# Kernel optimization log

Hardware: AMD Instinct MI355X
Metric: run time of the kernel (lower is better)

## Reference

```python
import jax, jax.numpy as jnp
import numpy as np

B, T = 128, 64
N_IN, H1, H2, N_OUT = 2048, 2048, 1024, 128
BETA = 0.95
THRESH = 1.0  # snn.Leaky default threshold


def spike(x):
    # Heaviside firing function (forward of snntorch ATan surrogate)
    return (x > 0).astype(x.dtype)


def setup_inputs() -> dict:
    key = jax.random.key(0)
    ks = jax.random.split(key, 5)

    def linear_params(k, fan_in, fan_out):
        k1, k2 = jax.random.split(k)
        bound = 1.0 / np.sqrt(fan_in)  # torch nn.Linear default init
        W = jax.random.uniform(k1, (fan_out, fan_in), minval=-bound, maxval=bound, dtype=jnp.float32)
        b = jax.random.uniform(k2, (fan_out,), minval=-bound, maxval=bound, dtype=jnp.float32)
        return W, b

    W0, b0 = linear_params(ks[0], N_IN, N_IN)
    W1, b1 = linear_params(ks[1], N_IN, H1)
    W2, b2 = linear_params(ks[2], H1, H2)
    W3, b3 = linear_params(ks[3], H2, N_OUT)
    x = jax.random.normal(ks[4], (B, T, N_IN), dtype=jnp.float32)
    return {"x": x, "W0": W0, "b0": b0, "W1": W1, "b1": b1,
            "W2": W2, "b2": b2, "W3": W3, "b3": b3}


def _lif(cur, mem):
    # snntorch Leaky (reset_mechanism='subtract'): reset computed from incoming mem
    reset = spike(mem - THRESH)
    mem_new = BETA * mem + cur - reset * THRESH
    spk = spike(mem_new - THRESH)
    return spk, mem_new


def reference(x, W0, b0, W1, b1, W2, b2, W3, b3):
    Bb = x.shape[0]
    dt = x.dtype
    mems0 = (jnp.zeros((Bb, N_IN), dt), jnp.zeros((Bb, H1), dt),
             jnp.zeros((Bb, H2), dt), jnp.zeros((Bb, N_OUT), dt))
    x_tbf = jnp.swapaxes(x, 0, 1)  # [T, B, N_IN]

    def step(carry, x_t):
        m0, m1, m2, m3 = carry
        s0, m0 = _lif(x_t @ W0.T + b0, m0)
        s1, m1 = _lif(s0 @ W1.T + b1, m1)
        s2, m2 = _lif(s1 @ W2.T + b2, m2)
        s3, m3 = _lif(s2 @ W3.T + b3, m3)
        return (m0, m1, m2, m3), (s3, m3)

    _, (spk3, mem3) = jax.lax.scan(step, mems0, x_tbf)
    # [T, B, N_OUT] -> [B, T, N_OUT]
    return jnp.swapaxes(spk3, 0, 1), jnp.swapaxes(mem3, 0, 1)
```

## Files before the change

### kernel.cpp

```cpp
#include <hip/hip_runtime.h>
#include <cstddef>
#include <cstdint>


#define BETA 0.95f

static constexpr int B_ = 128;
static constexpr int T_ = 64;
static constexpr int M_ = B_ * T_;
static constexpr int NOUT = 128;

typedef __bf16 bf16x8 __attribute__((ext_vector_type(8)));
typedef _Float16 f16x8 __attribute__((ext_vector_type(8)));
typedef float f32x4 __attribute__((ext_vector_type(4)));
typedef ushort u16x8 __attribute__((ext_vector_type(8)));

__device__ __forceinline__ ushort f32_bf16_rne(float f) {
  uint32_t u = __float_as_uint(f);
  uint32_t r = u + 0x7FFFu + ((u >> 16) & 1u);
  return (ushort)(r >> 16);
}
__device__ __forceinline__ float bf16_f32(ushort h) {
  return __uint_as_float(((uint32_t)h) << 16);
}
__device__ __forceinline__ ushort h2u(_Float16 h) {
  union { _Float16 h; ushort u; } v; v.h = h; return v.u;
}
__device__ __forceinline__ _Float16 u2h(ushort u) {
  union { ushort u; _Float16 h; } v; v.u = u; return v.h;
}

__global__ __launch_bounds__(256) void split2_f16(
    const float* __restrict__ S, ushort* __restrict__ oh,
    ushort* __restrict__ ol, int K, int nslots)
{
  int g = blockIdx.x * 256 + threadIdx.x;
  if (g >= nslots) return;
  int spr = K >> 3;
  int row = g / spr;
  int sl = g - row * spr;
  int kb = sl >> 3;
  int slot = sl & 7;
  int pslot = (slot & 4) | ((slot & 3) ^ ((row >> 1) & 3));
  const float* src = S + (size_t)row * K + (kb << 6) + (slot << 3);
  size_t dst = (size_t)row * K + (kb << 6) + (pslot << 3);
  u16x8 vh, vl;
#pragma unroll
  for (int i = 0; i < 8; ++i) {
    float f = src[i];
    _Float16 h = (_Float16)f;
    float hf = (float)h;
    if (fabsf(hf) < 6.103515625e-05f) { h = (_Float16)0.0f; hf = 0.0f; }
    float l = (f - hf) * 4096.0f;
    vh[i] = h2u(h);
    vl[i] = h2u((_Float16)l);
  }
  *reinterpret_cast<u16x8*>(oh + dst) = vh;
  *reinterpret_cast<u16x8*>(ol + dst) = vl;
}

__global__ __launch_bounds__(256) void split3_swz(
    const float* __restrict__ S, ushort* __restrict__ o1,
    ushort* __restrict__ o2, ushort* __restrict__ o3,
    int K, int nslots)
{
  int g = blockIdx.x * 256 + threadIdx.x;
  if (g >= nslots) return;
  int spr = K >> 3;
  int row = g / spr;
  int sl = g - row * spr;
  int kb = sl >> 3;
  int slot = sl & 7;
  int pslot = slot ^ (row & 7);
  const float* src = S + (size_t)row * K + (kb << 6) + (slot << 3);
  size_t dst = (size_t)row * K + (kb << 6) + (pslot << 3);
  u16x8 v1, v2, v3;
#pragma unroll
  for (int i = 0; i < 8; ++i) {
    float f = src[i];
    ushort h1 = f32_bf16_rne(f);
    float r = f - bf16_f32(h1);
    ushort h2 = f32_bf16_rne(r);
    float r2 = r - bf16_f32(h2);
    ushort h3 = f32_bf16_rne(r2);
    v1[i] = h1; v2[i] = h2; v3[i] = h3;
  }
  *reinterpret_cast<u16x8*>(o1 + dst) = v1;
  *reinterpret_cast<u16x8*>(o2 + dst) = v2;
  *reinterpret_cast<u16x8*>(o3 + dst) = v3;
}

template<int NP, int FMT>
__global__ __launch_bounds__(512) void gemm_mainL(
    const ushort* __restrict__ A0p, const ushort* __restrict__ A1p,
    const ushort* __restrict__ Bh0, const ushort* __restrict__ Bl0,
    const ushort* __restrict__ Bh1, const ushort* __restrict__ Bl1,
    int K, int N,
    const float* __restrict__ bias, ushort* __restrict__ spk)
{
  __shared__ __align__(16) ushort lds[67584];

  const int tid = threadIdx.x;
  const int lane = tid & 63;
  const int wid = tid >> 6;
  const int wm = wid >> 1;
  const int wn = wid & 1;
  const int lane15 = lane & 15;
  const int lhi = lane >> 4;
  const int sg2 = lhi ^ ((lane15 >> 1) & 3);

  int nwg = gridDim.x * gridDim.y;
  int bid = blockIdx.y * gridDim.x + blockIdx.x;
  int cpx = nwg >> 3;
  int sw = (bid & 7) * cpx + (bid >> 3);
  int bx = sw % gridDim.x, by = sw / gridDim.x;
  const int bm = by * 256, bn = bx * 128;

  const int sr2 = tid >> 2;
  const int sg = tid & 3;

  const ushort* Aps[2] = {A0p, (NP == 2) ? A1p : A0p};
  const ushort* Bhs[2] = {Bh0, (NP == 2) ? Bh1 : Bh0};
  const ushort* Bls[2] = {Bl0, (NP == 2) ? Bl1 : Bl0};

  auto stage = [&](int t1, int h, int d) {
    const int pn = t1 >> 5;
    const int k0 = (t1 & 31) * 64 + h * 32;
    const ushort* Ap = Aps[pn];
#pragma unroll
    for (int l = 0; l < 2; ++l) {
      int row = sr2 + l * 128;
      __builtin_amdgcn_global_load_lds(
          (const __attribute__((address_space(1))) void*)(Ap + (size_t)(bm + row) * K + k0 + sg * 8),
          (__attribute__((address_space(3))) void*)(lds + d * 16384 + h * 8192 + row * 32 + sg * 8),
          16, 0, 0);
    }
#pragma unroll
    for (int s = 0; s < 2; ++s) {
      const ushort* Bp = (s == 0) ? Bhs[pn] : Bls[pn];
      __builtin_amdgcn_global_load_lds(
          (const __attribute__((address_space(1))) void*)(Bp + (size_t)(bn + sr2) * K + k0 + sg * 8),
          (__attribute__((address_space(3))) void*)(lds + 32768 + ((d * 2 + h) * 2 + s) * 4096 + sr2 * 32 + sg * 8),
          16, 0, 0);
    }
  };

  f32x4 accM[4][4], accC[4][4];
#pragma unroll
  for (int i = 0; i < 4; ++i)
#pragma unroll
    for (int j = 0; j < 4; ++j) {
      accM[i][j] = (f32x4){0.f, 0.f, 0.f, 0.f};
      accC[i][j] = (f32x4){0.f, 0.f, 0.f, 0.f};
    }

  const int NT = NP * 32;

  stage(0, 0, 0);
  stage(0, 1, 0);
  asm volatile("s_waitcnt vmcnt(0)" ::: "memory");
  asm volatile("s_barrier" ::: "memory");

  for (int t = 0; t < NT; ++t) {
    const int d = t & 1;
    const int p = t >> 5;
    const int nb = (NP == 2 && p == 1) ? 1 : 2;
#pragma unroll
    for (int h = 0; h < 2; ++h) {
      f16x8 af[4];
      const ushort* Ab = lds + (d * 2 + h) * 8192;
#pragma unroll
      for (int i = 0; i < 4; ++i)
        af[i] = *(const f16x8*)(Ab + (wm * 64 + i * 16 + lane15) * 32 + sg2 * 8);

      if (t < NT - 1) {
        stage(t + 1, h, d ^ 1);
        asm volatile("s_waitcnt vmcnt(4)" ::: "memory");
      } else if (h == 0) {
        asm volatile("s_waitcnt vmcnt(0)" ::: "memory");
      }
      asm volatile("s_barrier" ::: "memory");

      __builtin_amdgcn_s_setprio(1);
#pragma unroll
      for (int s = 0; s < 2; ++s) {
        if (s < nb) {
          const ushort* Bb = lds + 32768 + ((d * 2 + h) * 2 + s) * 4096;
          f16x8 bf[4];
#pragma unroll
          for (int j = 0; j < 4; ++j)
            bf[j] = *(const f16x8*)(Bb + (wn * 64 + j * 16 + lane15) * 32 + sg2 * 8);
          if (p == 0 && s == 0) {
#pragma unroll
            for (int i = 0; i < 4; ++i)
#pragma unroll
              for (int j = 0; j < 4; ++j)
                accM[i][j] = __builtin_amdgcn_mfma_f32_16x16x32_f16(af[i], bf[j], accM[i][j], 0, 0, 0);
          } else {
#pragma unroll
            for (int i = 0; i < 4; ++i)
#pragma unroll
              for (int j = 0; j < 4; ++j)
                accC[i][j] = __builtin_amdgcn_mfma_f32_16x16x32_f16(af[i], bf[j], accC[i][j], 0, 0, 0);
          }
        }
      }
      __builtin_amdgcn_s_setprio(0);
      asm volatile("s_barrier" ::: "memory");
    }
  }

  asm volatile("s_waitcnt vmcnt(0)" ::: "memory");
  __syncthreads();

  float* curb = (float*)lds;
#pragma unroll
  for (int i = 0; i < 4; ++i) {
    int rl = wm * 64 + i * 16 + lhi * 4;
#pragma unroll
    for (int j = 0; j < 4; ++j) {
      int cl = wn * 64 + j * 16 + lane15;
      f32x4 vm = accM[i][j], vc = accC[i][j];
#pragma unroll
      for (int r = 0; r < 4; ++r)
        curb[(rl + r) * 132 + cl] = __fmaf_rn(vc[r], 2.44140625e-4f, vm[r]);
    }
  }
  __syncthreads();

  {
    int b2 = tid >> 7;
    int n = tid & 127;
    int cg = bn + n;
    float bv = bias[cg];
    int nb6 = cg >> 6;
    int sl = (cg >> 3) & 7;
    int nlow = cg & 7;
    const ushort one = FMT ? (ushort)0x3C00 : (ushort)0x3F80;
    float mem = 0.f;
    for (int t2 = 0; t2 < 64; ++t2) {
      float c = __fadd_rn(curb[(b2 * 64 + t2) * 132 + n], bv);
      float reset = ((mem - 1.0f) > 0.0f) ? 1.0f : 0.0f;
      mem = __fmul_rn(BETA, mem);
      mem = __fadd_rn(mem, c);
      mem = __fadd_rn(mem, -reset);
      ushort sv = ((mem - 1.0f) > 0.0f) ? one : (ushort)0;
      int m = bm + b2 * 64 + t2;
      int ps = FMT ? ((sl & 4) | ((sl & 3) ^ ((m >> 1) & 3)))
                   : (sl ^ (m & 7));
      spk[(size_t)m * N + (nb6 << 6) + (ps << 3) + nlow] = sv;
    }
  }
}

__global__ __launch_bounds__(256) void gemm_seg_lif(
    const ushort* __restrict__ A0,
    const ushort* __restrict__ B0, const ushort* __restrict__ B1,
    const ushort* __restrict__ B2,
    const float* __restrict__ bias,
    float* __restrict__ spk_out, float* __restrict__ mem_out)
{
  __shared__ ushort As[128 * 64];
  __shared__ ushort Bs[128 * 64];
  __shared__ float curb[128 * 132];

  const int tid = threadIdx.x;
  const int lane = tid & 63;
  const int wid = tid >> 6;
  const int wr = wid >> 1, wc = wid & 1;
  const int lane15 = lane & 15;
  const int lhi = lane >> 4;
  const int rswz = lane15 & 7;
  const int lrow = lane >> 3, lslot = lane & 7;

  int nwg = gridDim.x * gridDim.y;
  int bid = blockIdx.y * gridDim.x + blockIdx.x;
  int cpx = nwg >> 3;
  int sw = (bid & 7) * cpx + (bid >> 3);
  int bx = sw % gridDim.x, by = sw / gridDim.x;
  const int bm = by * 128, bn = bx * 128;

  f32x4 accM[4][4], accC[4][4];
#pragma unroll
  for (int i = 0; i < 4; ++i)
#pragma unroll
    for (int j = 0; j < 4; ++j) {
      accM[i][j] = (f32x4){0.f, 0.f, 0.f, 0.f};
      accC[i][j] = (f32x4){0.f, 0.f, 0.f, 0.f};
    }

  const bool isA = (wid < 2);
  ushort* lbase = isA ? As : Bs;
  const int rowbase0 = isA ? bm : bn;
  const int chunk0 = (wid & 1) * 8;

  for (int p = 0; p < 3; ++p) {
    const ushort* Bp = (p == 0) ? B0 : ((p == 1) ? B1 : B2);
    const ushort* gsrc = isA ? A0 : Bp;
    for (int k0 = 0; k0 < 1024; k0 += 64) {
      __syncthreads();
#pragma unroll
      for (int c = 0; c < 8; ++c) {
        int chunk = chunk0 + c;
        int row = chunk * 8 + lrow;
        const ushort* g = gsrc + (size_t)(rowbase0 + row) * 1024 + k0 + (lslot << 3);
        __builtin_amdgcn_global_load_lds(
            (const __attribute__((address_space(1))) void*)(g),
            (__attribute__((address_space(3))) void*)(lbase + chunk * 512),
            16, 0, 0);
      }
      __syncthreads();
#pragma unroll
      for (int kk = 0; kk < 2; ++kk) {
        int sp = ((kk << 2) | lhi) ^ rswz;
        bf16x8 af[4], bg[4];
#pragma unroll
        for (int i = 0; i < 4; ++i)
          af[i] = *(const bf16x8*)(As + (wr * 64 + i * 16 + lane15) * 64 + sp * 8);
#pragma unroll
        for (int j = 0; j < 4; ++j)
          bg[j] = *(const bf16x8*)(Bs + (wc * 64 + j * 16 + lane15) * 64 + sp * 8);
        if (p == 0) {
#pragma unroll
          for (int i = 0; i < 4; ++i)
#pragma unroll
            for (int j = 0; j < 4; ++j)
              accM[i][j] = __builtin_amdgcn_mfma_f32_16x16x32_bf16(af[i], bg[j], accM[i][j], 0, 0, 0);
        } else {
#pragma unroll
          for (int i = 0; i < 4; ++i)
#pragma unroll
            for (int j = 0; j < 4; ++j)
              accC[i][j] = __builtin_amdgcn_mfma_f32_16x16x32_bf16(af[i], bg[j], accC[i][j], 0, 0, 0);
        }
      }
    }
  }

  __syncthreads();
#pragma unroll
  for (int j = 0; j < 4; ++j) {
    int cl = wc * 64 + j * 16 + lane15;
#pragma unroll
    for (int i = 0; i < 4; ++i) {
      int rl = wr * 64 + i * 16 + lhi * 4;
      f32x4 vm = accM[i][j], vc = accC[i][j];
#pragma unroll
      for (int r = 0; r < 4; ++r)
        curb[(rl + r) * 132 + cl] = vm[r] + vc[r];
    }
  }
  __syncthreads();

  {
    int b2 = tid >> 7;
    int n = tid & 127;
    float bv = bias[bn + n];
    float mem = 0.f;
    for (int t2 = 0; t2 < 64; ++t2) {
      float c = __fadd_rn(curb[(b2 * 64 + t2) * 132 + n], bv);
      float reset = ((mem - 1.0f) > 0.0f) ? 1.0f : 0.0f;
      mem = __fmul_rn(BETA, mem);
      mem = __fadd_rn(mem, c);
      mem = __fadd_rn(mem, -reset);
      int m = bm + b2 * 64 + t2;
      size_t idx = (size_t)m * 128 + bn + n;
      spk_out[idx] = ((mem - 1.0f) > 0.0f) ? 1.0f : 0.0f;
      mem_out[idx] = mem;
    }
  }
}

extern "C" void kernel_launch(void* const* d_in, const int* in_sizes, int n_in,
                              void* d_out, int out_size, void* d_ws, size_t ws_size,
                              hipStream_t stream)
{
  const float* x  = (const float*)d_in[0];
  const float* W0 = (const float*)d_in[1];
  const float* b0 = (const float*)d_in[2];
  const float* W1 = (const float*)d_in[3];
  const float* b1 = (const float*)d_in[4];
  const float* W2 = (const float*)d_in[5];
  const float* b2 = (const float*)d_in[6];
  const float* W3 = (const float*)d_in[7];
  const float* b3 = (const float*)d_in[8];
  float* out = (float*)d_out;

  char* ws = (char*)d_ws;
  size_t off = 0;
  auto take = [&](size_t bytes) -> char* {
    char* p = ws + off;
    off += (bytes + 255) & ~(size_t)255;
    return p;
  };

  ushort* w0h = (ushort*)take((size_t)2048 * 2048 * 2);
  ushort* w0l = (ushort*)take((size_t)2048 * 2048 * 2);
  ushort* w1h = (ushort*)take((size_t)2048 * 2048 * 2);
  ushort* w1l = (ushort*)take((size_t)2048 * 2048 * 2);
  ushort* w2h = (ushort*)take((size_t)1024 * 2048 * 2);
  ushort* w2l = (ushort*)take((size_t)1024 * 2048 * 2);
  ushort* w3s[3];
  for (int i = 0; i < 3; ++i) w3s[i] = (ushort*)take((size_t)128 * 1024 * 2);
  ushort* xh = (ushort*)take((size_t)M_ * 2048 * 2);
  ushort* xl = (ushort*)take((size_t)M_ * 2048 * 2);
  ushort* s0 = (ushort*)take((size_t)M_ * 2048 * 2);
  ushort* s1 = xh;
  ushort* s2 = xl;

  dim3 blk(256);
  dim3 fblk(512);

  {
    int ns = 2048 * 2048 / 8;
    split2_f16<<<(ns + 255) / 256, blk, 0, stream>>>(W0, w0h, w0l, 2048, ns);
    split2_f16<<<(ns + 255) / 256, blk, 0, stream>>>(W1, w1h, w1l, 2048, ns);
    ns = 1024 * 2048 / 8;
    split2_f16<<<(ns + 255) / 256, blk, 0, stream>>>(W2, w2h, w2l, 2048, ns);
    ns = 128 * 1024 / 8;
    split3_swz<<<(ns + 255) / 256, blk, 0, stream>>>(W3, w3s[0], w3s[1], w3s[2], 1024, ns);
    ns = M_ * 2048 / 8;
    split2_f16<<<(ns + 255) / 256, blk, 0, stream>>>(x, xh, xl, 2048, ns);
  }

  {
    dim3 grid(2048 / 128, M_ / 256);
    gemm_mainL<2, 1><<<grid, fblk, 0, stream>>>(
        xh, xl, w0h, w0l, w0h, w0h, 2048, 2048, b0, s0);
  }
  {
    dim3 grid(2048 / 128, M_ / 256);
    gemm_mainL<1, 1><<<grid, fblk, 0, stream>>>(
        s0, s0, w1h, w1l, w1h, w1l, 2048, 2048, b1, s1);
  }
  {
    dim3 grid(1024 / 128, M_ / 256);
    gemm_mainL<1, 0><<<grid, fblk, 0, stream>>>(
        s1, s1, w2h, w2l, w2h, w2l, 2048, 1024, b2, s2);
  }
  {
    float* spk3 = out;
    float* mem3 = out + (size_t)M_ * NOUT;
    gemm_seg_lif<<<dim3(1, 64), blk, 0, stream>>>(s2, w3s[0], w3s[1], w3s[2], b3, spk3, mem3);
  }
}
```

Baseline: 478.0 us.

## Double-buffer LDS fragment reads in registers to overlap with MFMA

Restructures the GEMM main loop so the A/B fragments for the next half-tile are read from LDS into a second register set while MFMAs run on the current set. Each k-step is unrolled into two explicit halves with ping-pong fragment arrays, and the first fragments are preloaded before the loop. The aim is to hide LDS read latency behind matrix math. The cost is a larger live register set (two full fragment buffers on top of 128 accumulator registers), which may reduce occupancy or cause spills. There is also one redundant fragment read on the final iteration.

```diff
diff --git a/kernel.cpp b/kernel.cpp
--- a/kernel.cpp
+++ b/kernel.cpp
@@ -145,6 +145,22 @@
     }
   };
 
+  auto read_af = [&](int dd, int hh, f16x8* af) {
+    const ushort* Ab = lds + (dd * 2 + hh) * 8192;
+#pragma unroll
+    for (int i = 0; i < 4; ++i)
+      af[i] = *(const f16x8*)(Ab + (wm * 64 + i * 16 + lane15) * 32 + sg2 * 8);
+  };
+  auto read_bf = [&](int dd, int hh, f16x8* bf) {
+#pragma unroll
+    for (int s = 0; s < 2; ++s) {
+      const ushort* Bb = lds + 32768 + ((dd * 2 + hh) * 2 + s) * 4096;
+#pragma unroll
+      for (int j = 0; j < 4; ++j)
+        bf[s * 4 + j] = *(const f16x8*)(Bb + (wn * 64 + j * 16 + lane15) * 32 + sg2 * 8);
+    }
+  };
+
   f32x4 accM[4][4], accC[4][4];
 #pragma unroll
   for (int i = 0; i < 4; ++i)
@@ -161,53 +177,74 @@
   asm volatile("s_waitcnt vmcnt(0)" ::: "memory");
   asm volatile("s_barrier" ::: "memory");
 
+  f16x8 afA[4], bfA[8], afB[4], bfB[8];
+  read_af(0, 0, afA);
+  read_bf(0, 0, bfA);
+
   for (int t = 0; t < NT; ++t) {
     const int d = t & 1;
     const int p = t >> 5;
     const int nb = (NP == 2 && p == 1) ? 1 : 2;
-#pragma unroll
-    for (int h = 0; h < 2; ++h) {
-      f16x8 af[4];
-      const ushort* Ab = lds + (d * 2 + h) * 8192;
-#pragma unroll
-      for (int i = 0; i < 4; ++i)
-        af[i] = *(const f16x8*)(Ab + (wm * 64 + i * 16 + lane15) * 32 + sg2 * 8);
-
-      if (t < NT - 1) {
-        stage(t + 1, h, d ^ 1);
-        asm volatile("s_waitcnt vmcnt(4)" ::: "memory");
-      } else if (h == 0) {
-        asm volatile("s_waitcnt vmcnt(0)" ::: "memory");
-      }
-      asm volatile("s_barrier" ::: "memory");
-
-      __builtin_amdgcn_s_setprio(1);
-#pragma unroll
-      for (int s = 0; s < 2; ++s) {
-        if (s < nb) {
-          const ushort* Bb = lds + 32768 + ((d * 2 + h) * 2 + s) * 4096;
-          f16x8 bf[4];
-#pragma unroll
-          for (int j = 0; j < 4; ++j)
-            bf[j] = *(const f16x8*)(Bb + (wn * 64 + j * 16 + lane15) * 32 + sg2 * 8);
-          if (p == 0 && s == 0) {
-#pragma unroll
-            for (int i = 0; i < 4; ++i)
-#pragma unroll
-              for (int j = 0; j < 4; ++j)
-                accM[i][j] = __builtin_amdgcn_mfma_f32_16x16x32_f16(af[i], bf[j], accM[i][j], 0, 0, 0);
-          } else {
-#pragma unroll
-            for (int i = 0; i < 4; ++i)
-#pragma unroll
-              for (int j = 0; j < 4; ++j)
-                accC[i][j] = __builtin_amdgcn_mfma_f32_16x16x32_f16(af[i], bf[j], accC[i][j], 0, 0, 0);
-          }
+
+    if (t < NT - 1) {
+      stage(t + 1, 0, d ^ 1);
+      asm volatile("s_waitcnt vmcnt(4)" ::: "memory");
+    } else {
+      asm volatile("s_waitcnt vmcnt(0)" ::: "memory");
+    }
+    asm volatile("s_barrier" ::: "memory");
+    read_af(d, 1, afB);
+    read_bf(d, 1, bfB);
+    __builtin_amdgcn_s_setprio(1);
+#pragma unroll
+    for (int s = 0; s < 2; ++s) {
+      if (s < nb) {
+        if (p == 0 && s == 0) {
+#pragma unroll
+          for (int i = 0; i < 4; ++i)
+#pragma unroll
+            for (int j = 0; j < 4; ++j)
+              accM[i][j] = __builtin_amdgcn_mfma_f32_16x16x32_f16(afA[i], bfA[s * 4 + j], accM[i][j], 0, 0, 0);
+        } else {
+#pragma unroll
+          for (int i = 0; i < 4; ++i)
+#pragma unroll
+            for (int j = 0; j < 4; ++j)
+              accC[i][j] = __builtin_amdgcn_mfma_f32_16x16x32_f16(afA[i], bfA[s * 4 + j], accC[i][j], 0, 0, 0);
         }
       }
-      __builtin_amdgcn_s_setprio(0);
-      asm volatile("s_barrier" ::: "memory");
-    }
+    }
+    __builtin_amdgcn_s_setprio(0);
+    asm volatile("s_barrier" ::: "memory");
+
+    if (t < NT - 1) {
+      stage(t + 1, 1, d ^ 1);
+      asm volatile("s_waitcnt vmcnt(4)" ::: "memory");
+    }
+    asm volatile("s_barrier" ::: "memory");
+    read_af(d ^ 1, 0, afA);
+    read_bf(d ^ 1, 0, bfA);
+    __builtin_amdgcn_s_setprio(1);
+#pragma unroll
+    for (int s = 0; s < 2; ++s) {
+      if (s < nb) {
+        if (p == 0 && s == 0) {
+#pragma unroll
+          for (int i = 0; i < 4; ++i)
+#pragma unroll
+            for (int j = 0; j < 4; ++j)
+              accM[i][j] = __builtin_amdgcn_mfma_f32_16x16x32_f16(afB[i], bfB[s * 4 + j], accM[i][j], 0, 0, 0);
+        } else {
+#pragma unroll
+          for (int i = 0; i < 4; ++i)
+#pragma unroll
+            for (int j = 0; j < 4; ++j)
+              accC[i][j] = __builtin_amdgcn_mfma_f32_16x16x32_f16(afB[i], bfB[s * 4 + j], accC[i][j], 0, 0, 0);
+        }
+      }
+    }
+    __builtin_amdgcn_s_setprio(0);
+    asm volatile("s_barrier" ::: "memory");
   }
 
   asm volatile("s_waitcnt vmcnt(0)" ::: "memory");
```

Result: slower. 1.467 ms (+206.8%).
